# Kernel tuning notes

Hardware: AMD Instinct MI355X
Metric: run time of the kernel (lower is better)

Reference implementation:

```python
import jax, jax.numpy as jnp
import numpy as np

IN_FEATURES = 1024
OUT_FEATURES = 256
BATCH = 131072
EPS = 1e-4


def setup_inputs() -> dict:
    key = jax.random.key(0)
    kx, kw, kb = jax.random.split(key, 3)
    x = jax.random.normal(kx, (BATCH, IN_FEATURES), dtype=jnp.float32)
    # nn.Linear default init: U(-1/sqrt(in), 1/sqrt(in)) for both W and b
    bound = 1.0 / np.sqrt(IN_FEATURES)
    W = jax.random.uniform(kw, (OUT_FEATURES, IN_FEATURES), dtype=jnp.float32, minval=-bound, maxval=bound)
    b = jax.random.uniform(kb, (OUT_FEATURES,), dtype=jnp.float32, minval=-bound, maxval=bound)
    return {"x": x, "W": W, "b": b}


def reference(x, W, b):
    # L2-normalize each row (dim=1), matching x / (||x||_2 + 1e-4)
    norm = jnp.sqrt(jnp.sum(x * x, axis=1, keepdims=True))
    x_dir = x / (norm + EPS)
    # Linear: x_dir @ W^T + b, then ReLU
    h = jnp.einsum('bi,oi->bo', x_dir, W) + b
    return jax.nn.relu(h)
```

## Files before the change

kernel.cpp:

```cpp
#include <hip/hip_runtime.h>


#define IN_F   1024
#define OUT_F  256
#define BATCH  131072
#define BM     64
#define BK     32
#define NKT    32
#define EPSV   1e-4f

typedef __attribute__((ext_vector_type(8))) __bf16 bf16x8;
typedef __attribute__((ext_vector_type(4))) __bf16 bf16x4;
typedef __attribute__((ext_vector_type(4))) float  f32x4;

__device__ __forceinline__ void gload_lds16(const void* g, void* lds) {
  __builtin_amdgcn_global_load_lds(
      (const __attribute__((address_space(1))) void*)g,
      (__attribute__((address_space(3))) void*)lds, 16, 0, 0);
}

#define VM_WAIT(N) do { asm volatile("s_waitcnt vmcnt(" #N ")" ::: "memory"); \
                        __builtin_amdgcn_sched_barrier(0); } while (0)

__global__ void wconv_kernel(const float* __restrict__ W, __bf16* __restrict__ Wb) {
  const int t = blockIdx.x * blockDim.x + threadIdx.x;
  const float4 v = reinterpret_cast<const float4*>(W)[t];
  bf16x4 h;
  h[0] = (__bf16)v.x; h[1] = (__bf16)v.y; h[2] = (__bf16)v.z; h[3] = (__bf16)v.w;
  reinterpret_cast<bf16x4*>(Wb)[t] = h;
}

__global__ __launch_bounds__(512, 4)
void ffl_kernel(const float* __restrict__ x, const __bf16* __restrict__ Wb,
                const float* __restrict__ bias, float* __restrict__ out) {
  __shared__ __align__(16) char smem[73984];
  char* Abuf[3] = {smem, smem + 8192, smem + 16384};
  char* Bbuf[3] = {smem + 24576, smem + 40960, smem + 57344};

  const int tid  = threadIdx.x;
  const int lane = tid & 63;
  const int wave = tid >> 6;
  const int wr   = wave >> 2;
  const int wc   = wave & 3;
  const int rm   = lane & 15;
  const int q    = lane >> 4;
  const size_t block_row = (size_t)blockIdx.x * BM;

  const int arow = 8 * wave + (lane >> 3);
  const int asg  = (lane & 7) ^ (arow & 7);
  const float* aSrc = x + (block_row + arow) * IN_F + asg * 4;
  const int aDstOff = wave * 1024;

  int   brow[2]; const __bf16* bSrc[2]; int bDstOff[2];
  #pragma unroll
  for (int i = 0; i < 2; ++i) {
    const int c = 2 * wave + i;
    brow[i] = c * 16 + (lane >> 2);
    const int sg = (lane & 3) ^ ((brow[i] >> 1) & 3);
    bSrc[i] = Wb + (size_t)brow[i] * IN_F + sg * 8;
    bDstOff[i] = c * 1024;
  }

  f32x4 acc[2][4];
  #pragma unroll
  for (int m = 0; m < 2; ++m)
    #pragma unroll
    for (int n = 0; n < 4; ++n)
      acc[m][n] = (f32x4){0.f, 0.f, 0.f, 0.f};

  float ssq0 = 0.f, ssq1 = 0.f;

  auto stage = [&](int buf, int kt) {
    gload_lds16(aSrc + kt * BK, Abuf[buf] + aDstOff);
    gload_lds16(bSrc[0] + kt * BK, Bbuf[buf] + bDstOff[0]);
    gload_lds16(bSrc[1] + kt * BK, Bbuf[buf] + bDstOff[1]);
  };

  stage(0, 0);
  stage(1, 1);
  VM_WAIT(3);
  __builtin_amdgcn_s_barrier();

  #pragma unroll
  for (int kt = 0; kt < NKT; ++kt) {
    const int cur = kt % 3;
    if (kt + 2 < NKT) stage((kt + 2) % 3, kt + 2);

    bf16x8 aF[2];
    #pragma unroll
    for (int m = 0; m < 2; ++m) {
      const int ra = wr * 32 + m * 16 + rm;
      const char* ab = Abuf[cur] + ra * 128;
      const int sw = ra & 7;
      const f32x4 lo = *reinterpret_cast<const f32x4*>(ab + ((2 * q)     ^ sw) * 16);
      const f32x4 hi = *reinterpret_cast<const f32x4*>(ab + ((2 * q + 1) ^ sw) * 16);
      float& ssq = m ? ssq1 : ssq0;
      ssq += lo[0]*lo[0] + lo[1]*lo[1] + lo[2]*lo[2] + lo[3]*lo[3]
           + hi[0]*hi[0] + hi[1]*hi[1] + hi[2]*hi[2] + hi[3]*hi[3];
      bf16x8 a;
      a[0]=(__bf16)lo[0]; a[1]=(__bf16)lo[1]; a[2]=(__bf16)lo[2]; a[3]=(__bf16)lo[3];
      a[4]=(__bf16)hi[0]; a[5]=(__bf16)hi[1]; a[6]=(__bf16)hi[2]; a[7]=(__bf16)hi[3];
      aF[m] = a;
    }

    #pragma unroll
    for (int n = 0; n < 4; ++n) {
      const int rb = wc * 64 + n * 16 + rm;
      const bf16x8 bF = *reinterpret_cast<const bf16x8*>(
          Bbuf[cur] + rb * 64 + (q ^ ((rb >> 1) & 3)) * 16);
      acc[0][n] = __builtin_amdgcn_mfma_f32_16x16x32_bf16(aF[0], bF, acc[0][n], 0, 0, 0);
      acc[1][n] = __builtin_amdgcn_mfma_f32_16x16x32_bf16(aF[1], bF, acc[1][n], 0, 0, 0);
    }

    if (kt + 2 < NKT) { VM_WAIT(3); } else { VM_WAIT(0); }
    __builtin_amdgcn_s_barrier();
  }

  ssq0 += __shfl_xor(ssq0, 16); ssq0 += __shfl_xor(ssq0, 32);
  ssq1 += __shfl_xor(ssq1, 16); ssq1 += __shfl_xor(ssq1, 32);
  float* norms = reinterpret_cast<float*>(smem + 73728);
  if (wc == 0 && q == 0) {
    norms[wr * 32 + rm]      = 1.0f / (sqrtf(ssq0) + EPSV);
    norms[wr * 32 + 16 + rm] = 1.0f / (sqrtf(ssq1) + EPSV);
  }
  __syncthreads();

  float* stg = reinterpret_cast<float*>(smem);
  const int col0 = wc * 64 + rm;
  #pragma unroll
  for (int n = 0; n < 4; ++n) {
    const float bn = bias[col0 + n * 16];
    #pragma unroll
    for (int m = 0; m < 2; ++m) {
      #pragma unroll
      for (int j = 0; j < 4; ++j) {
        const int lr = wr * 32 + m * 16 + q * 4 + j;
        stg[lr * 260 + col0 + n * 16] = fmaxf(acc[m][n][j] * norms[lr] + bn, 0.f);
      }
    }
  }
  __syncthreads();

  const int r = tid >> 3, p = tid & 7;
  const float* srow = stg + r * 260;
  float* orow = out + (block_row + r) * OUT_F;
  #pragma unroll
  for (int i = 0; i < 8; ++i) {
    const int f = i * 8 + p;
    const f32x4 v = *reinterpret_cast<const f32x4*>(srow + f * 4);
    *reinterpret_cast<f32x4*>(orow + f * 4) = v;
  }
}

extern "C" void kernel_launch(void* const* d_in, const int* in_sizes, int n_in,
                              void* d_out, int out_size, void* d_ws, size_t ws_size,
                              hipStream_t stream) {
  const float* x = (const float*)d_in[0];
  const float* W = (const float*)d_in[1];
  const float* b = (const float*)d_in[2];
  float* out = (float*)d_out;
  __bf16* Wb = (__bf16*)d_ws;

  wconv_kernel<<<(OUT_F * IN_F / 4) / 256, 256, 0, stream>>>(W, Wb);
  ffl_kernel<<<BATCH / BM, 512, 0, stream>>>(x, Wb, b, out);
}
```

Measured before the change: 200.4 us.

## Double block row tile to 128 and stage x in 64-wide k chunks

After: 183.4 us. 8.5% less time.

```diff
diff --git a/kernel.cpp b/kernel.cpp
--- a/kernel.cpp
+++ b/kernel.cpp
@@ -4,8 +4,7 @@
 #define IN_F   1024
 #define OUT_F  256
 #define BATCH  131072
-#define BM     64
-#define BK     32
+#define BM     128
 #define NKT    32
 #define EPSV   1e-4f
 
@@ -30,12 +29,12 @@
   reinterpret_cast<bf16x4*>(Wb)[t] = h;
 }
 
-__global__ __launch_bounds__(512, 4)
+__global__ __launch_bounds__(1024, 4)
 void ffl_kernel(const float* __restrict__ x, const __bf16* __restrict__ Wb,
                 const float* __restrict__ bias, float* __restrict__ out) {
-  __shared__ __align__(16) char smem[73984];
-  char* Abuf[3] = {smem, smem + 8192, smem + 16384};
-  char* Bbuf[3] = {smem + 24576, smem + 40960, smem + 57344};
+  __shared__ __align__(16) char smem[147968];
+  char* const Ab[3] = {smem, smem + 32768, smem + 65536};
+  char* const Bb[3] = {smem + 98304, smem + 114688, smem + 131072};
 
   const int tid  = threadIdx.x;
   const int lane = tid & 63;
@@ -46,20 +45,19 @@
   const int q    = lane >> 4;
   const size_t block_row = (size_t)blockIdx.x * BM;
 
-  const int arow = 8 * wave + (lane >> 3);
-  const int asg  = (lane & 7) ^ (arow & 7);
-  const float* aSrc = x + (block_row + arow) * IN_F + asg * 4;
-  const int aDstOff = wave * 1024;
-
-  int   brow[2]; const __bf16* bSrc[2]; int bDstOff[2];
+  const float* aSrc[2]; int aDst[2];
   #pragma unroll
   for (int i = 0; i < 2; ++i) {
-    const int c = 2 * wave + i;
-    brow[i] = c * 16 + (lane >> 2);
-    const int sg = (lane & 3) ^ ((brow[i] >> 1) & 3);
-    bSrc[i] = Wb + (size_t)brow[i] * IN_F + sg * 8;
-    bDstOff[i] = c * 1024;
+    const int c   = 2 * wave + i;
+    const int row = 4 * c + (lane >> 4);
+    const int s   = (lane & 15) ^ (row & 7);
+    aSrc[i] = x + (block_row + row) * IN_F + s * 4;
+    aDst[i] = c * 1024;
   }
+  const int brow = 16 * wave + (lane >> 2);
+  const int bs   = (lane & 3) ^ ((brow >> 1) & 3);
+  const __bf16* bSrc = Wb + (size_t)brow * IN_F + bs * 8;
+  const int bDst = wave * 1024;
 
   f32x4 acc[2][4];
   #pragma unroll
@@ -70,30 +68,38 @@
 
   float ssq0 = 0.f, ssq1 = 0.f;
 
-  auto stage = [&](int buf, int kt) {
-    gload_lds16(aSrc + kt * BK, Abuf[buf] + aDstOff);
-    gload_lds16(bSrc[0] + kt * BK, Bbuf[buf] + bDstOff[0]);
-    gload_lds16(bSrc[1] + kt * BK, Bbuf[buf] + bDstOff[1]);
+  auto stageA = [&](int g) {
+    gload_lds16(aSrc[0] + g * 64, Ab[g % 3] + aDst[0]);
+    gload_lds16(aSrc[1] + g * 64, Ab[g % 3] + aDst[1]);
+  };
+  auto stageB = [&](int kt) {
+    gload_lds16(bSrc + kt * 32, Bb[kt % 3] + bDst);
   };
 
-  stage(0, 0);
-  stage(1, 1);
+  stageA(0);
+  stageB(0);
+  stageA(1);
+  stageB(1);
   VM_WAIT(3);
   __builtin_amdgcn_s_barrier();
 
   #pragma unroll
   for (int kt = 0; kt < NKT; ++kt) {
-    const int cur = kt % 3;
-    if (kt + 2 < NKT) stage((kt + 2) % 3, kt + 2);
+    if (kt + 2 < NKT) stageB(kt + 2);
+    if ((kt & 1) == 0 && (kt / 2 + 2) < 16) stageA(kt / 2 + 2);
+
+    const char* abuf = Ab[(kt >> 1) % 3];
+    const char* bbuf = Bb[kt % 3];
+    const int   gb   = (kt & 1) * 8 + 2 * q;
 
     bf16x8 aF[2];
     #pragma unroll
     for (int m = 0; m < 2; ++m) {
       const int ra = wr * 32 + m * 16 + rm;
-      const char* ab = Abuf[cur] + ra * 128;
+      const char* ab = abuf + ra * 256;
       const int sw = ra & 7;
-      const f32x4 lo = *reinterpret_cast<const f32x4*>(ab + ((2 * q)     ^ sw) * 16);
-      const f32x4 hi = *reinterpret_cast<const f32x4*>(ab + ((2 * q + 1) ^ sw) * 16);
+      const f32x4 lo = *reinterpret_cast<const f32x4*>(ab + ((gb)     ^ sw) * 16);
+      const f32x4 hi = *reinterpret_cast<const f32x4*>(ab + ((gb + 1) ^ sw) * 16);
       float& ssq = m ? ssq1 : ssq0;
       ssq += lo[0]*lo[0] + lo[1]*lo[1] + lo[2]*lo[2] + lo[3]*lo[3]
            + hi[0]*hi[0] + hi[1]*hi[1] + hi[2]*hi[2] + hi[3]*hi[3];
@@ -107,18 +113,20 @@
     for (int n = 0; n < 4; ++n) {
       const int rb = wc * 64 + n * 16 + rm;
       const bf16x8 bF = *reinterpret_cast<const bf16x8*>(
-          Bbuf[cur] + rb * 64 + (q ^ ((rb >> 1) & 3)) * 16);
+          bbuf + rb * 64 + (q ^ ((rb >> 1) & 3)) * 16);
       acc[0][n] = __builtin_amdgcn_mfma_f32_16x16x32_bf16(aF[0], bF, acc[0][n], 0, 0, 0);
       acc[1][n] = __builtin_amdgcn_mfma_f32_16x16x32_bf16(aF[1], bF, acc[1][n], 0, 0, 0);
     }
 
-    if (kt + 2 < NKT) { VM_WAIT(3); } else { VM_WAIT(0); }
+    if (kt < 28)      { VM_WAIT(3); }
+    else if (kt < 30) { VM_WAIT(1); }
+    else              { VM_WAIT(0); }
     __builtin_amdgcn_s_barrier();
   }
 
   ssq0 += __shfl_xor(ssq0, 16); ssq0 += __shfl_xor(ssq0, 32);
   ssq1 += __shfl_xor(ssq1, 16); ssq1 += __shfl_xor(ssq1, 32);
-  float* norms = reinterpret_cast<float*>(smem + 73728);
+  float* norms = reinterpret_cast<float*>(smem + 147456);
   if (wc == 0 && q == 0) {
     norms[wr * 32 + rm]      = 1.0f / (sqrtf(ssq0) + EPSV);
     norms[wr * 32 + 16 + rm] = 1.0f / (sqrtf(ssq1) + EPSV);
@@ -162,5 +170,5 @@
   __bf16* Wb = (__bf16*)d_ws;
 
   wconv_kernel<<<(OUT_F * IN_F / 4) / 256, 256, 0, stream>>>(W, Wb);
-  ffl_kernel<<<BATCH / BM, 512, 0, stream>>>(x, Wb, b, out);
+  ffl_kernel<<<BATCH / BM, 1024, 0, stream>>>(x, Wb, b, out);
 }
```

## Load W fragments directly from global, shrink LDS to double-buffered A only

Applied to the files above, without the earlier changes.

Result: slower. 358.7 us (+79.0%).

```diff
diff --git a/kernel.cpp b/kernel.cpp
--- a/kernel.cpp
+++ b/kernel.cpp
@@ -19,9 +19,6 @@
       (__attribute__((address_space(3))) void*)lds, 16, 0, 0);
 }
 
-#define VM_WAIT(N) do { asm volatile("s_waitcnt vmcnt(" #N ")" ::: "memory"); \
-                        __builtin_amdgcn_sched_barrier(0); } while (0)
-
 __global__ void wconv_kernel(const float* __restrict__ W, __bf16* __restrict__ Wb) {
   const int t = blockIdx.x * blockDim.x + threadIdx.x;
   const float4 v = reinterpret_cast<const float4*>(W)[t];
@@ -30,12 +27,11 @@
   reinterpret_cast<bf16x4*>(Wb)[t] = h;
 }
 
-__global__ __launch_bounds__(512, 4)
+__global__ __launch_bounds__(512, 2)
 void ffl_kernel(const float* __restrict__ x, const __bf16* __restrict__ Wb,
                 const float* __restrict__ bias, float* __restrict__ out) {
-  __shared__ __align__(16) char smem[73984];
-  char* Abuf[3] = {smem, smem + 8192, smem + 16384};
-  char* Bbuf[3] = {smem + 24576, smem + 40960, smem + 57344};
+  __shared__ __align__(16) char smem[34048];
+  char* const Ab[2] = {smem, smem + 8192};
 
   const int tid  = threadIdx.x;
   const int lane = tid & 63;
@@ -49,17 +45,14 @@
   const int arow = 8 * wave + (lane >> 3);
   const int asg  = (lane & 7) ^ (arow & 7);
   const float* aSrc = x + (block_row + arow) * IN_F + asg * 4;
-  const int aDstOff = wave * 1024;
+  const int aDst = wave * 1024;
 
-  int   brow[2]; const __bf16* bSrc[2]; int bDstOff[2];
+  const __bf16* bp = Wb + (size_t)(wc * 64 + rm) * IN_F + q * 8;
+
+  const int col0 = wc * 64 + rm;
+  float bn[4];
   #pragma unroll
-  for (int i = 0; i < 2; ++i) {
-    const int c = 2 * wave + i;
-    brow[i] = c * 16 + (lane >> 2);
-    const int sg = (lane & 3) ^ ((brow[i] >> 1) & 3);
-    bSrc[i] = Wb + (size_t)brow[i] * IN_F + sg * 8;
-    bDstOff[i] = c * 1024;
-  }
+  for (int n = 0; n < 4; ++n) bn[n] = bias[col0 + n * 16];
 
   f32x4 acc[2][4];
   #pragma unroll
@@ -70,27 +63,25 @@
 
   float ssq0 = 0.f, ssq1 = 0.f;
 
-  auto stage = [&](int buf, int kt) {
-    gload_lds16(aSrc + kt * BK, Abuf[buf] + aDstOff);
-    gload_lds16(bSrc[0] + kt * BK, Bbuf[buf] + bDstOff[0]);
-    gload_lds16(bSrc[1] + kt * BK, Bbuf[buf] + bDstOff[1]);
-  };
-
-  stage(0, 0);
-  stage(1, 1);
-  VM_WAIT(3);
-  __builtin_amdgcn_s_barrier();
+  gload_lds16(aSrc, Ab[0] + aDst);
+  __syncthreads();
 
   #pragma unroll
   for (int kt = 0; kt < NKT; ++kt) {
-    const int cur = kt % 3;
-    if (kt + 2 < NKT) stage((kt + 2) % 3, kt + 2);
+    const int cur = kt & 1;
+    if (kt + 1 < NKT)
+      gload_lds16(aSrc + (kt + 1) * BK, Ab[cur ^ 1] + aDst);
+
+    bf16x8 bF[4];
+    #pragma unroll
+    for (int n = 0; n < 4; ++n)
+      bF[n] = *reinterpret_cast<const bf16x8*>(bp + (size_t)n * 16 * IN_F + kt * BK);
 
     bf16x8 aF[2];
     #pragma unroll
     for (int m = 0; m < 2; ++m) {
       const int ra = wr * 32 + m * 16 + rm;
-      const char* ab = Abuf[cur] + ra * 128;
+      const char* ab = Ab[cur] + ra * 128;
       const int sw = ra & 7;
       const f32x4 lo = *reinterpret_cast<const f32x4*>(ab + ((2 * q)     ^ sw) * 16);
       const f32x4 hi = *reinterpret_cast<const f32x4*>(ab + ((2 * q + 1) ^ sw) * 16);
@@ -105,20 +96,16 @@
 
     #pragma unroll
     for (int n = 0; n < 4; ++n) {
-      const int rb = wc * 64 + n * 16 + rm;
-      const bf16x8 bF = *reinterpret_cast<const bf16x8*>(
-          Bbuf[cur] + rb * 64 + (q ^ ((rb >> 1) & 3)) * 16);
-      acc[0][n] = __builtin_amdgcn_mfma_f32_16x16x32_bf16(aF[0], bF, acc[0][n], 0, 0, 0);
-      acc[1][n] = __builtin_amdgcn_mfma_f32_16x16x32_bf16(aF[1], bF, acc[1][n], 0, 0, 0);
+      acc[0][n] = __builtin_amdgcn_mfma_f32_16x16x32_bf16(aF[0], bF[n], acc[0][n], 0, 0, 0);
+      acc[1][n] = __builtin_amdgcn_mfma_f32_16x16x32_bf16(aF[1], bF[n], acc[1][n], 0, 0, 0);
     }
 
-    if (kt + 2 < NKT) { VM_WAIT(3); } else { VM_WAIT(0); }
-    __builtin_amdgcn_s_barrier();
+    __syncthreads();
   }
 
   ssq0 += __shfl_xor(ssq0, 16); ssq0 += __shfl_xor(ssq0, 32);
   ssq1 += __shfl_xor(ssq1, 16); ssq1 += __shfl_xor(ssq1, 32);
-  float* norms = reinterpret_cast<float*>(smem + 73728);
+  float* norms = reinterpret_cast<float*>(smem + 33792);
   if (wc == 0 && q == 0) {
     norms[wr * 32 + rm]      = 1.0f / (sqrtf(ssq0) + EPSV);
     norms[wr * 32 + 16 + rm] = 1.0f / (sqrtf(ssq1) + EPSV);
@@ -126,29 +113,32 @@
   __syncthreads();
 
   float* stg = reinterpret_cast<float*>(smem);
-  const int col0 = wc * 64 + rm;
+  const int r = tid >> 3, p = tid & 7;
+  float* orow = out + (block_row + r) * OUT_F;
   #pragma unroll
-  for (int n = 0; n < 4; ++n) {
-    const float bn = bias[col0 + n * 16];
-    #pragma unroll
-    for (int m = 0; m < 2; ++m) {
+  for (int half = 0; half < 2; ++half) {
+    if ((wc >> 1) == half) {
+      const int cl = (wc & 1) * 64 + rm;
       #pragma unroll
-      for (int j = 0; j < 4; ++j) {
-        const int lr = wr * 32 + m * 16 + q * 4 + j;
-        stg[lr * 260 + col0 + n * 16] = fmaxf(acc[m][n][j] * norms[lr] + bn, 0.f);
+      for (int n = 0; n < 4; ++n) {
+        #pragma unroll
+        for (int m = 0; m < 2; ++m) {
+          #pragma unroll
+          for (int j = 0; j < 4; ++j) {
+            const int lr = wr * 32 + m * 16 + q * 4 + j;
+            stg[lr * 132 + cl + n * 16] = fmaxf(acc[m][n][j] * norms[lr] + bn[n], 0.f);
+          }
+        }
       }
     }
-  }
-  __syncthreads();
-
-  const int r = tid >> 3, p = tid & 7;
-  const float* srow = stg + r * 260;
-  float* orow = out + (block_row + r) * OUT_F;
-  #pragma unroll
-  for (int i = 0; i < 8; ++i) {
-    const int f = i * 8 + p;
-    const f32x4 v = *reinterpret_cast<const f32x4*>(srow + f * 4);
-    *reinterpret_cast<f32x4*>(orow + f * 4) = v;
+    __syncthreads();
+    #pragma unroll
+    for (int i = 0; i < 4; ++i) {
+      const int f = i * 8 + p;
+      const f32x4 v = *reinterpret_cast<const f32x4*>(stg + r * 132 + f * 4);
+      *reinterpret_cast<f32x4*>(orow + half * 128 + f * 4) = v;
+    }
+    __syncthreads();
   }
 }
 
```
